# Performance work log

Measured on AMD Instinct MI355X. Metric: run time of the kernel, lower is better.

## Reference

```python
import jax, jax.numpy as jnp
import numpy as np

B, O, M, H, E = 32, 64, 128, 4, 64  # batch, num_obj, memory_len, heads, embed


def setup_inputs() -> dict:
    key = jax.random.key(0)
    ks = jax.random.split(key, 10)
    s = 1.0 / np.sqrt(E)
    return {
        "query": jax.random.normal(ks[0], (B, O, E), jnp.float32),
        "context": jax.random.normal(ks[1], (B, M, E), jnp.float32),
        "memory": jax.random.normal(ks[2], (B, M, E), jnp.float32),
        "W_ch": jax.random.normal(ks[3], (E, H * E), jnp.float32) * s,
        "b_ch": jax.random.normal(ks[4], (H * E,), jnp.float32) * s,
        "w_logit": jax.random.normal(ks[5], (E,), jnp.float32) * s,
        "b_logit": jax.random.normal(ks[6], (1,), jnp.float32) * s,
        "W_rh": jax.random.normal(ks[7], (H * E, E), jnp.float32) * (1.0 / np.sqrt(H * E)),
        "b_rh": jax.random.normal(ks[8], (E,), jnp.float32) * (1.0 / np.sqrt(H * E)),
        "temp": jnp.float32(1.0),
    }


def reference(query, context, memory, W_ch, b_ch, w_logit, b_logit, W_rh, b_rh, temp):
    # create heads: [B,O,E] -> [B,O,H,E]
    q = (query @ W_ch + b_ch).reshape(B, O, H, E)
    # broadcast add query heads and context over memory axis: [B,O,M,H,E]
    qc = jnp.tanh(context[:, None, :, None, :] + q[:, :, None, :, :])
    # logit projection -> [B,O,M,H]
    logits = jnp.einsum("bomhe,e->bomh", qc, w_logit) + b_logit[0]
    # softmax over memory axis (dim=2)
    probs = jax.nn.softmax(logits / temp, axis=2)
    # weighted sum of memory over M: [B,O,H,E]
    heads = jnp.einsum("bomh,bme->bohe", probs, memory)
    heads = jax.nn.leaky_relu(heads, negative_slope=0.01)
    out = heads.reshape(B, O, H * E) @ W_rh + b_rh
    return out
```

## Files before the change

### kernel.cpp

```cpp
#include <hip/hip_runtime.h>
#include <hip/hip_fp16.h>

#define B 32
#define O 64
#define M 128
#define H 4
#define E 64
#define SC 2.88539008177792681f
#define LOG2E 1.44269504088896341f
#define MSTR 65

#if __has_builtin(__builtin_amdgcn_exp2f)
#define EXP2F(x) __builtin_amdgcn_exp2f(x)
#else
#define EXP2F(x) __exp2f(x)
#endif

__device__ __forceinline__ float rl(float v, int lane) {
    return __uint_as_float(__builtin_amdgcn_readlane(__float_as_uint(v), lane));
}
__device__ __forceinline__ unsigned pk2h(float a, float b) {
    return (unsigned)__half_as_ushort(__float2half_rn(a)) |
           ((unsigned)__half_as_ushort(__float2half_rn(b)) << 16);
}

__global__ __launch_bounds__(256) void prep_kernel(
    const float* __restrict__ query, const float* __restrict__ context,
    const float* __restrict__ memory, const float* __restrict__ W_ch,
    const float* __restrict__ b_ch,
    __half* __restrict__ ctx_Eh, __half* __restrict__ mem_T, float* __restrict__ q_E)
{
    __shared__ float s[128 * 68];
    const int t = threadIdx.x, blk = blockIdx.x;

    if (blk < 64) {
        const int b = blk & 31;
        const bool is_ctx = blk < 32;
        const int e = t >> 2, mb = (t & 3) * 32;
        const float* src = (is_ctx ? context : memory) + b * (M * E);
        #pragma unroll
        for (int i = 0; i < 8; ++i) {
            int idx = i * 1024 + t * 4;
            float4 v = *(const float4*)(src + idx);
            *(float4*)(&s[(idx >> 6) * 68 + (idx & 63)]) = v;
        }
        __syncthreads();
        if (is_ctx) {
            uint4* dst = (uint4*)(ctx_Eh + (size_t)b * (E * M) + e * M + mb);
            #pragma unroll
            for (int qd = 0; qd < 4; ++qd) {
                unsigned u[4];
                #pragma unroll
                for (int k = 0; k < 4; ++k) {
                    int m0 = mb + qd * 8 + 2 * k;
                    float ea = fminf(EXP2F(SC * s[m0 * 68 + e]), 60000.f);
                    float eb = fminf(EXP2F(SC * s[(m0 + 1) * 68 + e]), 60000.f);
                    u[k] = pk2h(ea, eb);
                }
                dst[qd] = make_uint4(u[0], u[1], u[2], u[3]);
            }
        } else {
            uint4* dst = (uint4*)(mem_T + (size_t)b * (E * M) + e * M + mb);
            #pragma unroll
            for (int qd = 0; qd < 4; ++qd) {
                unsigned u[4];
                #pragma unroll
                for (int k = 0; k < 4; ++k) {
                    int m0 = mb + qd * 8 + 2 * k;
                    u[k] = pk2h(s[m0 * 68 + e], s[(m0 + 1) * 68 + e]);
                }
                dst[qd] = make_uint4(u[0], u[1], u[2], u[3]);
            }
        }
    } else {
        const int r0 = (blk - 64) * 4;
        s[t] = query[(r0 + (t & 3)) * 64 + (t >> 2)];
        __syncthreads();
        float bc = b_ch[t];
        float a0 = bc, a1 = bc, a2 = bc, a3 = bc;
        #pragma unroll 8
        for (int k = 0; k < 64; ++k) {
            float4 qv = *(const float4*)(&s[k * 4]);
            float wv = W_ch[k * 256 + t];
            a0 = fmaf(qv.x, wv, a0);
            a1 = fmaf(qv.y, wv, a1);
            a2 = fmaf(qv.z, wv, a2);
            a3 = fmaf(qv.w, wv, a3);
        }
        float* qa = q_E + (size_t)r0 * 256 + t;
        qa[0]   = EXP2F(SC * a0);
        qa[256] = EXP2F(SC * a1);
        qa[512] = EXP2F(SC * a2);
        qa[768] = EXP2F(SC * a3);
    }
}

__global__ __launch_bounds__(256) void attn_main(
    const __half* __restrict__ ctx_Eh, const __half* __restrict__ mem_T,
    const float* __restrict__ q_E, const float* __restrict__ w_logit,
    const float* __restrict__ b_logit, const float* __restrict__ temp,
    const float* __restrict__ W_rh, const float* __restrict__ b_rh,
    float* __restrict__ out)
{
    __shared__ __half s_E[E * M];
    __shared__ float  s_M[E * MSTR];
    __shared__ float  s_po0[4 * E];
    __shared__ float  s_po1[4 * E];

    const int t = threadIdx.x, lane = t & 63, w = t >> 6;
    const int bo0 = blockIdx.x * 2, bo1 = bo0 + 1, b = bo0 >> 6;

    {
        const uint4* g = (const uint4*)(ctx_Eh + (size_t)b * (E * M));
        uint4* l = (uint4*)s_E;
        #pragma unroll
        for (int p = 0; p < 4; ++p)
            l[p * 256 + t] = g[p * 256 + t];
    }
    {
        const uint2* g = (const uint2*)(mem_T + (size_t)b * (E * M));
        const int e = t >> 2, j0 = (t & 3) * 16;
        #pragma unroll
        for (int i = 0; i < 8; ++i) {
            uint2 v = g[e * 32 + (j0 >> 1) + i];
            s_M[e * MSTR + j0 + 2 * i]     = __uint_as_float(v.x);
            s_M[e * MSTR + j0 + 2 * i + 1] = __uint_as_float(v.y);
        }
    }
    const float wl  = w_logit[lane];
    const float qE0 = q_E[bo0 * 256 + t];
    const float qE1 = q_E[bo1 * 256 + t];
    float sumw = wl;
    #pragma unroll
    for (int sft = 1; sft < 64; sft <<= 1) sumw += __shfl_xor(sumw, sft);
    const float bl   = b_logit[0];
    const float lsc  = LOG2E / temp[0];
    const float base = (sumw + bl) * lsc;
    const float lsc2 = -2.0f * lsc;
    __syncthreads();

    float a00 = 0.f, a01 = 0.f, a10 = 0.f, a11 = 0.f;
    const __half2* Ep = (const __half2*)s_E;
    #pragma unroll 4
    for (int e = 0; e < 64; ++e) {
        float2 cf = __half22float2(Ep[e * 64 + lane]);
        float q0 = rl(qE0, e);
        float q1 = rl(qE1, e);
        float we = rl(wl, e);
        float t00 = fmaf(cf.x, q0, 1.0f);
        float t01 = fmaf(cf.y, q0, 1.0f);
        float t10 = fmaf(cf.x, q1, 1.0f);
        float t11 = fmaf(cf.y, q1, 1.0f);
        float r0 = __builtin_amdgcn_rcpf(t00 * t01);
        float r1 = __builtin_amdgcn_rcpf(t10 * t11);
        float w0 = we * r0;
        float w1 = we * r1;
        a00 = fmaf(w0, t01, a00);  a01 = fmaf(w0, t00, a01);
        a10 = fmaf(w1, t11, a10);  a11 = fmaf(w1, t10, a11);
    }

    float l00 = fmaf(lsc2, a00, base), l01 = fmaf(lsc2, a01, base);
    float l10 = fmaf(lsc2, a10, base), l11 = fmaf(lsc2, a11, base);
    float mx0 = fmaxf(l00, l01), mx1 = fmaxf(l10, l11);
    #pragma unroll
    for (int sft = 1; sft < 64; sft <<= 1) {
        mx0 = fmaxf(mx0, __shfl_xor(mx0, sft));
        mx1 = fmaxf(mx1, __shfl_xor(mx1, sft));
    }
    float e00 = EXP2F(l00 - mx0), e01 = EXP2F(l01 - mx0);
    float e10 = EXP2F(l10 - mx1), e11 = EXP2F(l11 - mx1);
    float s0 = e00 + e01, s1 = e10 + e11;
    #pragma unroll
    for (int sft = 1; sft < 64; sft <<= 1) {
        s0 += __shfl_xor(s0, sft);
        s1 += __shfl_xor(s1, sft);
    }
    float rs0 = __builtin_amdgcn_rcpf(s0), rs1 = __builtin_amdgcn_rcpf(s1);

    float h0 = 0.f, h1 = 0.f;
    {
        const float* mrow = &s_M[lane * MSTR];
        #pragma unroll 8
        for (int j = 0; j < 64; ++j) {
            __half2 mh = *(const __half2*)&mrow[j];
            float2 mv = __half22float2(mh);
            float p00 = rl(e00, j), p01 = rl(e01, j);
            float p10 = rl(e10, j), p11 = rl(e11, j);
            h0 = fmaf(p00, mv.x, h0); h0 = fmaf(p01, mv.y, h0);
            h1 = fmaf(p10, mv.x, h1); h1 = fmaf(p11, mv.y, h1);
        }
    }
    float hv0 = h0 * rs0;
    float hv1 = h1 * rs1;
    hv0 = (hv0 > 0.f) ? hv0 : 0.01f * hv0;
    hv1 = (hv1 > 0.f) ? hv1 : 0.01f * hv1;

    {
        float acc0 = 0.f, acc1 = 0.f;
        const float* Wp = W_rh + (w * 64) * 64 + lane;
        #pragma unroll 8
        for (int jj = 0; jj < 64; ++jj) {
            float wv = Wp[jj * 64];
            acc0 = fmaf(rl(hv0, jj), wv, acc0);
            acc1 = fmaf(rl(hv1, jj), wv, acc1);
        }
        s_po0[w * 64 + lane] = acc0;
        s_po1[w * 64 + lane] = acc1;
    }
    __syncthreads();
    if (t < 64) {
        float o = s_po0[t] + s_po0[64 + t] + s_po0[128 + t] + s_po0[192 + t] + b_rh[t];
        out[(size_t)bo0 * 64 + t] = o;
    } else if (t < 128) {
        int e2 = t - 64;
        float o = s_po1[e2] + s_po1[64 + e2] + s_po1[128 + e2] + s_po1[192 + e2] + b_rh[e2];
        out[(size_t)bo1 * 64 + e2] = o;
    }
}

extern "C" void kernel_launch(void* const* d_in, const int* in_sizes, int n_in,
                              void* d_out, int out_size, void* d_ws, size_t ws_size,
                              hipStream_t stream) {
    const float* query   = (const float*)d_in[0];
    const float* context = (const float*)d_in[1];
    const float* memory  = (const float*)d_in[2];
    const float* W_ch    = (const float*)d_in[3];
    const float* b_ch    = (const float*)d_in[4];
    const float* w_logit = (const float*)d_in[5];
    const float* b_logit = (const float*)d_in[6];
    const float* W_rh    = (const float*)d_in[7];
    const float* b_rh    = (const float*)d_in[8];
    const float* temp    = (const float*)d_in[9];
    float* out = (float*)d_out;

    __half* ctx_Eh  = (__half*)d_ws;
    __half* mem_T   = ctx_Eh + (size_t)B * E * M;
    float*  q_E     = (float*)(mem_T + (size_t)B * E * M);

    prep_kernel<<<576, 256, 0, stream>>>(query, context, memory, W_ch, b_ch,
                                         ctx_Eh, mem_T, q_E);
    attn_main<<<B * O / 2, 256, 0, stream>>>(ctx_Eh, mem_T, q_E, w_logit,
                                             b_logit, temp, W_rh, b_rh, out);
}
```

Baseline: 99.81 us.

## Fuse prep and attention kernels into a single kernel

```diff
diff --git a/kernel.cpp b/kernel.cpp
--- a/kernel.cpp
+++ b/kernel.cpp
@@ -8,7 +8,8 @@
 #define E 64
 #define SC 2.88539008177792681f
 #define LOG2E 1.44269504088896341f
-#define MSTR 65
+#define SSTR 68
+#define ESTR 65
 
 #if __has_builtin(__builtin_amdgcn_exp2f)
 #define EXP2F(x) __builtin_amdgcn_exp2f(x)
@@ -24,112 +25,52 @@
            ((unsigned)__half_as_ushort(__float2half_rn(b)) << 16);
 }
 
-__global__ __launch_bounds__(256) void prep_kernel(
-    const float* __restrict__ query, const float* __restrict__ context,
-    const float* __restrict__ memory, const float* __restrict__ W_ch,
+__global__ __launch_bounds__(256) void attn_fused(
+    const float* __restrict__ query,
+    const float* __restrict__ context,
+    const float* __restrict__ memory,
+    const float* __restrict__ W_ch,
     const float* __restrict__ b_ch,
-    __half* __restrict__ ctx_Eh, __half* __restrict__ mem_T, float* __restrict__ q_E)
-{
-    __shared__ float s[128 * 68];
-    const int t = threadIdx.x, blk = blockIdx.x;
-
-    if (blk < 64) {
-        const int b = blk & 31;
-        const bool is_ctx = blk < 32;
-        const int e = t >> 2, mb = (t & 3) * 32;
-        const float* src = (is_ctx ? context : memory) + b * (M * E);
-        #pragma unroll
-        for (int i = 0; i < 8; ++i) {
-            int idx = i * 1024 + t * 4;
-            float4 v = *(const float4*)(src + idx);
-            *(float4*)(&s[(idx >> 6) * 68 + (idx & 63)]) = v;
-        }
-        __syncthreads();
-        if (is_ctx) {
-            uint4* dst = (uint4*)(ctx_Eh + (size_t)b * (E * M) + e * M + mb);
-            #pragma unroll
-            for (int qd = 0; qd < 4; ++qd) {
-                unsigned u[4];
-                #pragma unroll
-                for (int k = 0; k < 4; ++k) {
-                    int m0 = mb + qd * 8 + 2 * k;
-                    float ea = fminf(EXP2F(SC * s[m0 * 68 + e]), 60000.f);
-                    float eb = fminf(EXP2F(SC * s[(m0 + 1) * 68 + e]), 60000.f);
-                    u[k] = pk2h(ea, eb);
-                }
-                dst[qd] = make_uint4(u[0], u[1], u[2], u[3]);
-            }
-        } else {
-            uint4* dst = (uint4*)(mem_T + (size_t)b * (E * M) + e * M + mb);
-            #pragma unroll
-            for (int qd = 0; qd < 4; ++qd) {
-                unsigned u[4];
-                #pragma unroll
-                for (int k = 0; k < 4; ++k) {
-                    int m0 = mb + qd * 8 + 2 * k;
-                    u[k] = pk2h(s[m0 * 68 + e], s[(m0 + 1) * 68 + e]);
-                }
-                dst[qd] = make_uint4(u[0], u[1], u[2], u[3]);
-            }
-        }
-    } else {
-        const int r0 = (blk - 64) * 4;
-        s[t] = query[(r0 + (t & 3)) * 64 + (t >> 2)];
-        __syncthreads();
-        float bc = b_ch[t];
-        float a0 = bc, a1 = bc, a2 = bc, a3 = bc;
-        #pragma unroll 8
-        for (int k = 0; k < 64; ++k) {
-            float4 qv = *(const float4*)(&s[k * 4]);
-            float wv = W_ch[k * 256 + t];
-            a0 = fmaf(qv.x, wv, a0);
-            a1 = fmaf(qv.y, wv, a1);
-            a2 = fmaf(qv.z, wv, a2);
-            a3 = fmaf(qv.w, wv, a3);
-        }
-        float* qa = q_E + (size_t)r0 * 256 + t;
-        qa[0]   = EXP2F(SC * a0);
-        qa[256] = EXP2F(SC * a1);
-        qa[512] = EXP2F(SC * a2);
-        qa[768] = EXP2F(SC * a3);
-    }
-}
-
-__global__ __launch_bounds__(256) void attn_main(
-    const __half* __restrict__ ctx_Eh, const __half* __restrict__ mem_T,
-    const float* __restrict__ q_E, const float* __restrict__ w_logit,
-    const float* __restrict__ b_logit, const float* __restrict__ temp,
-    const float* __restrict__ W_rh, const float* __restrict__ b_rh,
+    const float* __restrict__ w_logit,
+    const float* __restrict__ b_logit,
+    const float* __restrict__ W_rh,
+    const float* __restrict__ b_rh,
+    const float* __restrict__ temp,
     float* __restrict__ out)
 {
-    __shared__ __half s_E[E * M];
-    __shared__ float  s_M[E * MSTR];
-    __shared__ float  s_po0[4 * E];
-    __shared__ float  s_po1[4 * E];
+    __shared__ float    s_S[M * SSTR];
+    __shared__ unsigned s_E[E * ESTR];
+    __shared__ float    s_po0[4 * E];
+    __shared__ float    s_po1[4 * E];
 
     const int t = threadIdx.x, lane = t & 63, w = t >> 6;
     const int bo0 = blockIdx.x * 2, bo1 = bo0 + 1, b = bo0 >> 6;
 
     {
-        const uint4* g = (const uint4*)(ctx_Eh + (size_t)b * (E * M));
-        uint4* l = (uint4*)s_E;
-        #pragma unroll
-        for (int p = 0; p < 4; ++p)
-            l[p * 256 + t] = g[p * 256 + t];
-    }
-    {
-        const uint2* g = (const uint2*)(mem_T + (size_t)b * (E * M));
-        const int e = t >> 2, j0 = (t & 3) * 16;
+        const float* ctx = context + b * (M * E);
         #pragma unroll
         for (int i = 0; i < 8; ++i) {
-            uint2 v = g[e * 32 + (j0 >> 1) + i];
-            s_M[e * MSTR + j0 + 2 * i]     = __uint_as_float(v.x);
-            s_M[e * MSTR + j0 + 2 * i + 1] = __uint_as_float(v.y);
+            int idx = i * 1024 + t * 4;
+            float4 v = *(const float4*)(ctx + idx);
+            *(float4*)(&s_S[(idx >> 6) * SSTR + (idx & 63)]) = v;
         }
     }
-    const float wl  = w_logit[lane];
-    const float qE0 = q_E[bo0 * 256 + t];
-    const float qE1 = q_E[bo1 * 256 + t];
+    float qE0, qE1;
+    {
+        float qq0 = query[bo0 * E + lane];
+        float qq1 = query[bo1 * E + lane];
+        float acc0 = b_ch[t], acc1 = acc0;
+        const float* Wc = W_ch + t;
+        #pragma unroll 16
+        for (int k = 0; k < 64; ++k) {
+            float wv = Wc[k * 256];
+            acc0 = fmaf(rl(qq0, k), wv, acc0);
+            acc1 = fmaf(rl(qq1, k), wv, acc1);
+        }
+        qE0 = EXP2F(SC * acc0);
+        qE1 = EXP2F(SC * acc1);
+    }
+    const float wl = w_logit[lane];
     float sumw = wl;
     #pragma unroll
     for (int sft = 1; sft < 64; sft <<= 1) sumw += __shfl_xor(sumw, sft);
@@ -139,11 +80,33 @@
     const float lsc2 = -2.0f * lsc;
     __syncthreads();
 
+    {
+        const int e = lane, c0 = w * 16;
+        #pragma unroll
+        for (int k = 0; k < 16; ++k) {
+            int m0 = 2 * (c0 + k);
+            float ea = fminf(EXP2F(SC * s_S[m0 * SSTR + e]), 60000.f);
+            float eb = fminf(EXP2F(SC * s_S[(m0 + 1) * SSTR + e]), 60000.f);
+            s_E[e * ESTR + c0 + k] = pk2h(ea, eb);
+        }
+    }
+    __syncthreads();
+
+    {
+        const float* mem = memory + b * (M * E);
+        #pragma unroll
+        for (int i = 0; i < 8; ++i) {
+            int idx = i * 1024 + t * 4;
+            float4 v = *(const float4*)(mem + idx);
+            *(float4*)(&s_S[(idx >> 6) * SSTR + (idx & 63)]) = v;
+        }
+    }
+
     float a00 = 0.f, a01 = 0.f, a10 = 0.f, a11 = 0.f;
-    const __half2* Ep = (const __half2*)s_E;
     #pragma unroll 4
     for (int e = 0; e < 64; ++e) {
-        float2 cf = __half22float2(Ep[e * 64 + lane]);
+        __half2 c2 = *(const __half2*)&s_E[e * ESTR + lane];
+        float2 cf = __half22float2(c2);
         float q0 = rl(qE0, e);
         float q1 = rl(qE1, e);
         float we = rl(wl, e);
@@ -176,19 +139,17 @@
         s1 += __shfl_xor(s1, sft);
     }
     float rs0 = __builtin_amdgcn_rcpf(s0), rs1 = __builtin_amdgcn_rcpf(s1);
+    __syncthreads();
 
     float h0 = 0.f, h1 = 0.f;
-    {
-        const float* mrow = &s_M[lane * MSTR];
-        #pragma unroll 8
-        for (int j = 0; j < 64; ++j) {
-            __half2 mh = *(const __half2*)&mrow[j];
-            float2 mv = __half22float2(mh);
-            float p00 = rl(e00, j), p01 = rl(e01, j);
-            float p10 = rl(e10, j), p11 = rl(e11, j);
-            h0 = fmaf(p00, mv.x, h0); h0 = fmaf(p01, mv.y, h0);
-            h1 = fmaf(p10, mv.x, h1); h1 = fmaf(p11, mv.y, h1);
-        }
+    #pragma unroll 8
+    for (int j = 0; j < 64; ++j) {
+        float mv0 = s_S[(2 * j) * SSTR + lane];
+        float mv1 = s_S[(2 * j + 1) * SSTR + lane];
+        float p00 = rl(e00, j), p01 = rl(e01, j);
+        float p10 = rl(e10, j), p11 = rl(e11, j);
+        h0 = fmaf(p00, mv0, h0); h0 = fmaf(p01, mv1, h0);
+        h1 = fmaf(p10, mv0, h1); h1 = fmaf(p11, mv1, h1);
     }
     float hv0 = h0 * rs0;
     float hv1 = h1 * rs1;
@@ -233,12 +194,6 @@
     const float* temp    = (const float*)d_in[9];
     float* out = (float*)d_out;
 
-    __half* ctx_Eh  = (__half*)d_ws;
-    __half* mem_T   = ctx_Eh + (size_t)B * E * M;
-    float*  q_E     = (float*)(mem_T + (size_t)B * E * M);
-
-    prep_kernel<<<576, 256, 0, stream>>>(query, context, memory, W_ch, b_ch,
-                                         ctx_Eh, mem_T, q_E);
-    attn_main<<<B * O / 2, 256, 0, stream>>>(ctx_Eh, mem_T, q_E, w_logit,
-                                             b_logit, temp, W_rh, b_rh, out);
+    attn_fused<<<B * O / 2, 256, 0, stream>>>(query, context, memory, W_ch, b_ch,
+                                              w_logit, b_logit, W_rh, b_rh, temp, out);
 }
```

After: 100.1 us. About the same (+0.3%).
